# Kernel tuning notes

Measured on AMD Instinct MI355X. Metric: run time of the kernel, lower is better.

The kernel has to match this reference:

```python
import jax, jax.numpy as jnp
import numpy as np

B, S, D = 2, 2048, 2048
H, KVH, HD = 16, 4, 128
E, TOPK, FF = 8, 2, 4096
EPS = 1e-6
THETA = 1000000.0


def setup_inputs() -> dict:
    key = jax.random.key(0)
    ks = jax.random.split(key, 12)
    s = 0.02
    return {
        'hidden_states': jax.random.normal(ks[0], (B, S, D), jnp.float32),
        'attention_mask': jnp.ones((B, S), dtype=bool),
        'wq': jax.random.normal(ks[1], (D, H * HD), jnp.float32) * s,
        'wk': jax.random.normal(ks[2], (D, KVH * HD), jnp.float32) * s,
        'wv': jax.random.normal(ks[3], (D, KVH * HD), jnp.float32) * s,
        'wo': jax.random.normal(ks[4], (H * HD, D), jnp.float32) * s,
        'ln1_w': jnp.ones((D,), jnp.float32),
        'ln2_w': jnp.ones((D,), jnp.float32),
        'gate_w': jax.random.normal(ks[5], (D, E), jnp.float32) * s,
        'w_gate': jax.random.normal(ks[6], (E, D, FF), jnp.float32) * s,
        'w_up': jax.random.normal(ks[7], (E, D, FF), jnp.float32) * s,
        'w_down': jax.random.normal(ks[8], (E, FF, D), jnp.float32) * s,
    }


def rms_norm(x, w):
    xf = x.astype(jnp.float32)
    var = jnp.mean(jnp.square(xf), axis=-1, keepdims=True)
    return w * (xf * jax.lax.rsqrt(var + EPS)).astype(x.dtype)


def rotate_half(x):
    x1, x2 = x[..., : x.shape[-1] // 2], x[..., x.shape[-1] // 2 :]
    return jnp.concatenate((-x2, x1), axis=-1)


def attention(x, mask, wq, wk, wv, wo):
    q = (x @ wq).reshape(B, S, H, HD)
    k = (x @ wk).reshape(B, S, KVH, HD)
    v = (x @ wv).reshape(B, S, KVH, HD)
    # RoPE (fp32 freqs, as in MixtralRotaryEmbedding)
    inv_freq = 1.0 / (THETA ** (jnp.arange(0, HD, 2, dtype=jnp.float32) / HD))
    freqs = jnp.arange(S, dtype=jnp.float32)[:, None] * inv_freq[None, :]  # [S, HD/2]
    emb = jnp.concatenate([freqs, freqs], axis=-1)  # [S, HD]
    cos = jnp.cos(emb)[None, :, None, :]  # [1,S,1,HD]
    sin = jnp.sin(emb)[None, :, None, :]
    q = q * cos + rotate_half(q) * sin
    k = k * cos + rotate_half(k) * sin
    # GQA: repeat kv heads
    k = jnp.repeat(k, H // KVH, axis=2)
    v = jnp.repeat(v, H // KVH, axis=2)
    # faithful to source: keep-mask is triu(ones, k=1) (strictly-above-diagonal)
    causal = jnp.triu(jnp.ones((S, S), dtype=bool), k=1)
    combined = mask[:, None, None, :] & causal[None, None, :, :]  # [B,1,S,S]
    neg = jnp.finfo(jnp.float32).min
    bias = jnp.where(combined, 0.0, neg).astype(jnp.float32)
    scores = jnp.einsum('bqhd,bkhd->bhqk', q, k) * (HD ** -0.5) + bias
    attn = jax.nn.softmax(scores, axis=-1)
    out = jnp.einsum('bhqk,bkhd->bqhd', attn, v).reshape(B, S, H * HD)
    return out @ wo


def moe(x, gate_w, w_gate, w_up, w_down):
    # x: [T, D]
    T = x.shape[0]
    logits = x.astype(jnp.float32) @ gate_w  # fp32 router, [T, E]
    rw = jax.nn.softmax(logits, axis=-1)
    top_w, top_i = jax.lax.top_k(rw, TOPK)
    top_w = top_w / jnp.sum(top_w, axis=-1, keepdims=True)
    w_full = jnp.zeros((T, E), jnp.float32).at[jnp.arange(T)[:, None], top_i].set(top_w)
    out = jnp.zeros_like(x)
    for e in range(E):  # small fixed expert loop
        h = jax.nn.silu(x @ w_gate[e]) * (x @ w_up[e])
        out = out + w_full[:, e, None] * (h @ w_down[e])
    return out


def reference(hidden_states, attention_mask, wq, wk, wv, wo, ln1_w, ln2_w, gate_w, w_gate, w_up, w_down):
    residual = hidden_states
    h = rms_norm(hidden_states, ln1_w)
    h = residual + attention(h, attention_mask, wq, wk, wv, wo)
    residual = h
    h = rms_norm(h, ln2_w)
    m = moe(h.reshape(-1, D), gate_w, w_gate, w_up, w_down).reshape(B, S, D)
    return residual + m
```

## Files before the change

kernel.cpp:

```cpp
#include <hip/hip_runtime.h>
#include <cstdint>
#include <cstddef>


typedef unsigned short u16;
typedef __attribute__((ext_vector_type(8))) short short8;
typedef __attribute__((ext_vector_type(8))) _Float16 half8;
typedef __attribute__((ext_vector_type(8))) __bf16 bf16x8;
typedef __attribute__((ext_vector_type(4))) float f32x4;
typedef __attribute__((ext_vector_type(4))) u16 us4;
typedef __attribute__((ext_vector_type(4))) unsigned int u32x4;

__device__ __forceinline__ u16 f2bf(float f) {
  unsigned u = __builtin_bit_cast(unsigned, f);
  u += 0x7fffu + ((u >> 16) & 1u);
  return (u16)(u >> 16);
}
__device__ __forceinline__ void splitf16(float x, float scale, u16 &hi, u16 &lo) {
  float xs = x * scale;
  _Float16 h = (_Float16)xs;
  hi = __builtin_bit_cast(u16, h);
  _Float16 l = (_Float16)(xs - (float)h);
  lo = __builtin_bit_cast(u16, l);
}
__device__ __forceinline__ f32x4 mma_bf(short8 a, short8 b, f32x4 c) {
  return __builtin_amdgcn_mfma_f32_16x16x32_bf16(
      __builtin_bit_cast(bf16x8, a), __builtin_bit_cast(bf16x8, b), c, 0, 0, 0);
}
__device__ __forceinline__ f32x4 mma_h(short8 a, short8 b, f32x4 c) {
  return __builtin_amdgcn_mfma_f32_16x16x32_f16(
      __builtin_bit_cast(half8, a), __builtin_bit_cast(half8, b), c, 0, 0, 0);
}
__device__ __forceinline__ void gl16(const u16 *g, u16 *l) {
  __builtin_amdgcn_global_load_lds(
      (const __attribute__((address_space(1))) unsigned *)g,
      (__attribute__((address_space(3))) unsigned *)l, 16, 0, 0);
}

template <int OM>
__global__ __launch_bounds__(256) void k_trans(
    const float *__restrict__ src, u16 *__restrict__ d0, u16 *__restrict__ d1,
    int ld_src, int ld_dst, long long zhi, long long zlo, int zmod,
    long long dstz, int inter, float scale) {
  int z = blockIdx.z;
  src += (long long)(z / zmod) * zhi + (long long)(z % zmod) * zlo;
  d0 += (long long)z * dstz;
  if constexpr (OM == 1) d1 += (long long)z * dstz;
  int r0 = blockIdx.y * 64, c0 = blockIdx.x * 64;
  __shared__ float t[64][65];
  int tx = threadIdx.x;
  int rr = tx >> 4, cc = (tx & 15) * 4;
#pragma unroll
  for (int i = 0; i < 4; i++) {
    float4 v = *(const float4 *)(src + (size_t)(r0 + rr + i * 16) * ld_src + c0 + cc);
    t[rr + i * 16][cc] = v.x; t[rr + i * 16][cc + 1] = v.y;
    t[rr + i * 16][cc + 2] = v.z; t[rr + i * 16][cc + 3] = v.w;
  }
  __syncthreads();
#pragma unroll
  for (int i = 0; i < 4; i++) {
    int c = rr + i * 16;
    int f = c0 + c;
    int drow = (inter < 0) ? f : (((f >> 5) << 6) + (f & 31) + (inter << 5));
    size_t bo = (size_t)drow * ld_dst + r0 + cc;
    if constexpr (OM == 0) {
      us4 o;
#pragma unroll
      for (int j = 0; j < 4; j++) o[j] = f2bf(t[cc + j][c]);
      *(us4 *)(d0 + bo) = o;
    } else {
      us4 oh, ol;
#pragma unroll
      for (int j = 0; j < 4; j++) {
        u16 a, b; splitf16(t[cc + j][c], scale, a, b);
        oh[j] = a; ol[j] = b;
      }
      *(us4 *)(d0 + bo) = oh;
      *(us4 *)(d1 + bo) = ol;
    }
  }
}

__global__ __launch_bounds__(256) void k_rms(
    const float *__restrict__ x, const float *__restrict__ w,
    u16 *__restrict__ oh, u16 *__restrict__ ol, float scale16) {
  int row = blockIdx.x, tid = threadIdx.x;
  const float *xr = x + (size_t)row * 2048;
  float4 v0 = *(const float4 *)(xr + tid * 8);
  float4 v1 = *(const float4 *)(xr + tid * 8 + 4);
  float ss = v0.x * v0.x + v0.y * v0.y + v0.z * v0.z + v0.w * v0.w +
             v1.x * v1.x + v1.y * v1.y + v1.z * v1.z + v1.w * v1.w;
  __shared__ float red[256];
  red[tid] = ss;
  __syncthreads();
  for (int s = 128; s > 0; s >>= 1) {
    if (tid < s) red[tid] += red[tid + s];
    __syncthreads();
  }
  float sc = rsqrtf(red[0] * (1.0f / 2048.0f) + 1e-6f);
  float4 w0 = *(const float4 *)(w + tid * 8);
  float4 w1 = *(const float4 *)(w + tid * 8 + 4);
  float o[8] = {v0.x * sc * w0.x, v0.y * sc * w0.y, v0.z * sc * w0.z, v0.w * sc * w0.w,
                v1.x * sc * w1.x, v1.y * sc * w1.y, v1.z * sc * w1.z, v1.w * sc * w1.w};
  size_t bo = (size_t)row * 2048 + tid * 8;
  if (ol) {
    us4 h0, h1, l0, l1;
#pragma unroll
    for (int j = 0; j < 4; j++) {
      u16 a, b;
      splitf16(o[j], scale16, a, b); h0[j] = a; l0[j] = b;
      splitf16(o[j + 4], scale16, a, b); h1[j] = a; l1[j] = b;
    }
    *(us4 *)(oh + bo) = h0; *(us4 *)(oh + bo + 4) = h1;
    *(us4 *)(ol + bo) = l0; *(us4 *)(ol + bo + 4) = l1;
  } else {
    us4 a, b;
#pragma unroll
    for (int j = 0; j < 4; j++) { a[j] = f2bf(o[j]); b[j] = f2bf(o[j + 4]); }
    *(us4 *)(oh + bo) = a; *(us4 *)(oh + bo + 4) = b;
  }
}

__global__ void k_cs(float2 *__restrict__ cs) {
  int idx = blockIdx.x * 256 + threadIdx.x;
  int s = idx >> 6, i = idx & 63;
  double inv = exp2(-(double)i * (19.931568569324174 / 64.0));
  double ang = (double)s * inv;
  cs[idx] = make_float2((float)cos(ang), (float)sin(ang));
}

__global__ __launch_bounds__(256) void k_rope(
    const float *__restrict__ qkv, const float2 *__restrict__ cs,
    u16 *__restrict__ qh, u16 *__restrict__ ql,
    u16 *__restrict__ kh, u16 *__restrict__ kl) {
  int t = blockIdx.x, tid = threadIdx.x;
  int s = t & 2047;
  const float *bp = qkv + (size_t)t * 3072;
  for (int p = tid; p < 1024; p += 256) {
    int hh = p >> 6, i = p & 63;
    float2 c = cs[s * 64 + i];
    float x1 = bp[hh * 128 + i], x2 = bp[hh * 128 + 64 + i];
    float o1 = x1 * c.x - x2 * c.y, o2 = x2 * c.x + x1 * c.y;
    size_t b1 = (size_t)t * 2048 + hh * 128 + i;
    u16 a, b;
    splitf16(o1, 16.f, a, b); qh[b1] = a; ql[b1] = b;
    splitf16(o2, 16.f, a, b); qh[b1 + 64] = a; ql[b1 + 64] = b;
  }
  {
    int hh = tid >> 6, i = tid & 63;
    float2 c = cs[s * 64 + i];
    float x1 = bp[2048 + hh * 128 + i], x2 = bp[2048 + hh * 128 + 64 + i];
    float o1 = x1 * c.x - x2 * c.y, o2 = x2 * c.x + x1 * c.y;
    size_t b1 = (size_t)t * 512 + hh * 128 + i;
    u16 a, b;
    splitf16(o1, 16.f, a, b); kh[b1] = a; kl[b1] = b;
    splitf16(o2, 16.f, a, b); kh[b1 + 64] = a; kl[b1 + 64] = b;
  }
}

__global__ __launch_bounds__(256) void k_attn(
    const u16 *__restrict__ qh, const u16 *__restrict__ ql,
    const u16 *__restrict__ kh, const u16 *__restrict__ kl,
    const u16 *__restrict__ vh, const u16 *__restrict__ vl,
    u16 *__restrict__ oh, u16 *__restrict__ ol) {
  const int qt = blockIdx.x, kvh = blockIdx.y, b = blockIdx.z;
  const int q0 = qt * 16;
  const int tid = threadIdx.x, wid = tid >> 6, lane = tid & 63;
  const int h = kvh * 4 + wid;
  const int lr = lane & 15, g = lane >> 4, lk = g * 8;
  const float SC = 0.08838834764831845f * 1.44269504088896341f / 256.0f;

  __shared__ alignas(16) u16 KT[2][2][4096];
  __shared__ alignas(16) u16 VT[2][2][4096];
  __shared__ alignas(16) u16 Pb[4][2][512];

  short8 qfh[4], qfl[4];
  {
    size_t qo = (size_t)(b * 2048 + q0 + lr) * 2048 + h * 128 + lk;
#pragma unroll
    for (int c = 0; c < 4; c++) {
      qfh[c] = *(const short8 *)(qh + qo + c * 32);
      qfl[c] = *(const short8 *)(ql + qo + c * 32);
    }
  }
  f32x4 accO[8] = {};
  float m_r[4], l_r[4];
#pragma unroll
  for (int r = 0; r < 4; r++) { m_r[r] = -3.0e38f; l_r[r] = 0.f; }

  const int kv_start = (q0 == 2032) ? 0 : (((q0 + 1) >> 5) << 5);
  const int nIter = (2048 - kv_start) >> 5;

  const u16 *khp = kh + (size_t)(b * 2048) * 512 + kvh * 128;
  const u16 *klp = kl + (size_t)(b * 2048) * 512 + kvh * 128;
  const u16 *vhp = vh + ((size_t)(b * 4 + kvh) * 128) * 2048;
  const u16 *vlp = vl + ((size_t)(b * 4 + kvh) * 128) * 2048;

  auto stage = [&](int bf, int kv0) {
#pragma unroll
    for (int j = 0; j < 2; j++) {
      const int c0 = wid * 128 + j * 64;
      const int cc = c0 + lane;
      const int krow = cc >> 4, kcol = (cc & 15) ^ (krow & 7);
      const size_t kg = (size_t)(kv0 + krow) * 512 + kcol * 8;
      gl16(khp + kg, &KT[bf][0][c0 * 8]);
      gl16(klp + kg, &KT[bf][1][c0 * 8]);
      const int vd = cc >> 2, vi = (cc & 3) ^ (vd & 3);
      const size_t vg = (size_t)vd * 2048 + kv0 + vi * 8;
      gl16(vhp + vg, &VT[bf][0][c0 * 8]);
      gl16(vlp + vg, &VT[bf][1][c0 * 8]);
    }
  };

  stage(0, kv_start);
  __syncthreads();
  int buf = 0;
  for (int it = 0; it < nIter; it++) {
    const int kv0 = kv_start + (it << 5);
    if (it + 1 < nIter) stage(buf ^ 1, kv0 + 32);
    f32x4 s0 = {}, s1 = {};
    {
      const u16 *KhL = KT[buf][0], *KlL = KT[buf][1];
#pragma unroll
      for (int c = 0; c < 4; c++) {
        const int idx0 = lr * 128 + (((c * 4 + g) ^ (lr & 7)) << 3);
        const int idx1 = idx0 + 2048;
        short8 k0h = *(const short8 *)(KhL + idx0);
        short8 k0l = *(const short8 *)(KlL + idx0);
        short8 k1h = *(const short8 *)(KhL + idx1);
        short8 k1l = *(const short8 *)(KlL + idx1);
        s0 = mma_h(qfh[c], k0h, s0); s0 = mma_h(qfh[c], k0l, s0); s0 = mma_h(qfl[c], k0h, s0);
        s1 = mma_h(qfh[c], k1h, s1); s1 = mma_h(qfh[c], k1l, s1); s1 = mma_h(qfl[c], k1h, s1);
      }
    }
    const bool msk = (kv0 <= q0 + 15);
    float alpha[4];
#pragma unroll
    for (int r = 0; r < 4; r++) {
      float v0 = s0[r] * SC, v1 = s1[r] * SC;
      if (msk) {
        int rowq = q0 + g * 4 + r;
        if (kv0 + lr <= rowq) v0 = -3.0e38f;
        if (kv0 + 16 + lr <= rowq) v1 = -3.0e38f;
      }
      float mx = fmaxf(v0, v1);
#pragma unroll
      for (int o = 1; o < 16; o <<= 1) mx = fmaxf(mx, __shfl_xor(mx, o));
      float mn = fmaxf(m_r[r], mx);
      float p0 = exp2f(v0 - mn), p1 = exp2f(v1 - mn);
      float sum = p0 + p1;
#pragma unroll
      for (int o = 1; o < 16; o <<= 1) sum += __shfl_xor(sum, o);
      alpha[r] = exp2f(m_r[r] - mn);
      l_r[r] = l_r[r] * alpha[r] + sum;
      m_r[r] = mn;
      const int prow = g * 4 + r;
      {
        int c0l = lr, c1l = 16 + lr;
        int p0i = prow * 32 + ((c0l & 7) | ((((c0l >> 3) ^ g) & 3) << 3));
        int p1i = prow * 32 + ((c1l & 7) | ((((c1l >> 3) ^ g) & 3) << 3));
        u16 x, y;
        splitf16(p0, 16.f, x, y); Pb[wid][0][p0i] = x; Pb[wid][1][p0i] = y;
        splitf16(p1, 16.f, x, y); Pb[wid][0][p1i] = x; Pb[wid][1][p1i] = y;
      }
    }
#pragma unroll
    for (int nt = 0; nt < 8; nt++) {
      f32x4 t = accO[nt];
      t[0] *= alpha[0]; t[1] *= alpha[1]; t[2] *= alpha[2]; t[3] *= alpha[3];
      accO[nt] = t;
    }
    asm volatile("s_waitcnt lgkmcnt(0)" ::: "memory");
    const int pidx = lr * 32 + (((g ^ (lr >> 2)) & 3) << 3);
    short8 pfh = *(const short8 *)(&Pb[wid][0][pidx]);
    short8 pfl = *(const short8 *)(&Pb[wid][1][pidx]);
    {
      const u16 *VhL = VT[buf][0], *VlL = VT[buf][1];
#pragma unroll
      for (int nt = 0; nt < 8; nt++) {
        const int d = nt * 16 + lr;
        const int vidx = d * 32 + (((g ^ (d & 3)) & 3) << 3);
        short8 wfh = *(const short8 *)(VhL + vidx);
        short8 wfl = *(const short8 *)(VlL + vidx);
        f32x4 t = accO[nt];
        t = mma_h(pfh, wfh, t); t = mma_h(pfh, wfl, t); t = mma_h(pfl, wfh, t);
        accO[nt] = t;
      }
    }
    __syncthreads();
    buf ^= 1;
  }
  float inv[4];
#pragma unroll
  for (int r = 0; r < 4; r++) inv[r] = 1.0f / (l_r[r] * 256.0f);
#pragma unroll
  for (int nt = 0; nt < 8; nt++)
#pragma unroll
    for (int r = 0; r < 4; r++) {
      float v = accO[nt][r] * inv[r];
      size_t idx = (size_t)(b * 2048 + q0 + g * 4 + r) * 2048 + h * 128 + nt * 16 + lr;
      u16 x, y; splitf16(v, 16.f, x, y);
      oh[idx] = x; ol[idx] = y;
    }
}

template <int MODE>
__global__ __launch_bounds__(256) void k_gemm(
    const u16 *__restrict__ Ah, const u16 *__restrict__ Al,
    const u16 *__restrict__ Bh, const u16 *__restrict__ Bl,
    int M, int N, int K, int lda, int ldb, int ldc, float descale,
    float *__restrict__ outf, const float *__restrict__ resid) {
  const int tid = threadIdx.x;
  const int wid = tid >> 6, lane = tid & 63;
  const int wr = wid >> 1, wc = wid & 1;
  const int l15 = lane & 15, l4 = lane >> 4;
  const int n0 = blockIdx.x * 128, m0 = blockIdx.y * 128;
  __shared__ alignas(16) u16 AsH[4096], BsH[4096];
  __shared__ alignas(16) u16 AsL[4096], BsL[4096];
  const int r16 = lane >> 2, c8 = (lane & 3) << 3;
  int a0 = m0 + wid * 16 + r16, a1 = a0 + 64;
  const u16 *pa0 = Ah + (size_t)a0 * lda + c8;
  const u16 *pa1 = Ah + (size_t)a1 * lda + c8;
  const int b0 = n0 + wid * 16 + r16, b1 = b0 + 64;
  const u16 *pb0 = Bh + (size_t)b0 * ldb + c8;
  const u16 *pb1 = Bh + (size_t)b1 * ldb + c8;
  const u16 *qa0 = Al + (size_t)a0 * lda + c8;
  const u16 *qa1 = Al + (size_t)a1 * lda + c8;
  const u16 *qb0 = Bl + (size_t)b0 * ldb + c8;
  const u16 *qb1 = Bl + (size_t)b1 * ldb + c8;
  u16 *sa0 = AsH + wid * 512, *sa1 = AsH + 2048 + wid * 512;
  u16 *sb0 = BsH + wid * 512, *sb1 = BsH + 2048 + wid * 512;
  f32x4 acc[4][4] = {};
  const int fa = (wr * 64 + l15) * 32 + (l4 << 3);
  const int fb = (wc * 64 + l15) * 32 + (l4 << 3);
  for (int k0 = 0; k0 < K; k0 += 32) {
    gl16(pa0 + k0, sa0); gl16(pa1 + k0, sa1);
    gl16(pb0 + k0, sb0); gl16(pb1 + k0, sb1);
    gl16(qa0 + k0, AsL + wid * 512); gl16(qa1 + k0, AsL + 2048 + wid * 512);
    gl16(qb0 + k0, BsL + wid * 512); gl16(qb1 + k0, BsL + 2048 + wid * 512);
    __syncthreads();
    short8 ah[4], bh[4], al[4], bl[4];
#pragma unroll
    for (int i = 0; i < 4; i++) ah[i] = *(const short8 *)(AsH + fa + i * 512);
#pragma unroll
    for (int i = 0; i < 4; i++) bh[i] = *(const short8 *)(BsH + fb + i * 512);
#pragma unroll
    for (int i = 0; i < 4; i++) al[i] = *(const short8 *)(AsL + fa + i * 512);
#pragma unroll
    for (int i = 0; i < 4; i++) bl[i] = *(const short8 *)(BsL + fb + i * 512);
#pragma unroll
    for (int mi = 0; mi < 4; mi++)
#pragma unroll
      for (int ni = 0; ni < 4; ni++) {
        f32x4 c = acc[mi][ni];
        c = mma_h(ah[mi], bh[ni], c);
        c = mma_h(ah[mi], bl[ni], c);
        c = mma_h(al[mi], bh[ni], c);
        acc[mi][ni] = c;
      }
    __syncthreads();
  }
#pragma unroll
  for (int mi = 0; mi < 4; mi++)
#pragma unroll
    for (int q = 0; q < 4; q++) {
      int row = m0 + wr * 64 + l4 * 4 + mi * 16 + q;
      size_t rb = (size_t)row * ldc;
#pragma unroll
      for (int ni = 0; ni < 4; ni++) {
        int col = n0 + wc * 64 + ni * 16 + l15;
        float v = acc[mi][ni][q] * descale;
        if constexpr (MODE == 1) v += resid[rb + col];
        outf[rb + col] = v;
      }
    }
}

template <int MODE>
__global__ __launch_bounds__(512, 1) void k_gemm8(
    const u16 *__restrict__ A, const u16 *__restrict__ Ball,
    int N, int K, int lda, int ldb, int ldc,
    float *__restrict__ outf, u16 *__restrict__ outh,
    const int *__restrict__ offs, const int *__restrict__ counts,
    const int *__restrict__ row_token, const float *__restrict__ row_w) {
  const int e = blockIdx.z;
  const int seg = offs[e], cnt = counts[e];
  const int m0 = blockIdx.y * 256;
  if (m0 >= cnt) return;
  const int n0 = blockIdx.x * 256;
  const u16 *B = Ball + (size_t)e * (size_t)N * (size_t)ldb;
  const int tid = threadIdx.x, wid = tid >> 6, lane = tid & 63;
  const int wr = wid >> 2, wc = wid & 3;
  const int l15 = lane & 15, l4 = lane >> 4;

  __shared__ alignas(16) u16 Ls[4][2][8192];

  const u16 *pA[2], *pB[2];
#pragma unroll
  for (int j = 0; j < 2; j++) {
    int s = (wid * 2 + j) * 64 + lane;
    int row = s >> 2;
    int kc = (s & 3) ^ ((row >> 1) & 3);
    int ra = m0 + row; if (ra > cnt - 1) ra = cnt - 1;
    pA[j] = A + (size_t)(seg + ra) * lda + kc * 8;
    pB[j] = B + (size_t)(n0 + row) * ldb + kc * 8;
  }
  int offA[8], offB[4];
#pragma unroll
  for (int mi = 0; mi < 8; mi++) {
    int r = wr * 128 + mi * 16 + l15;
    offA[mi] = (r * 4 + (l4 ^ ((r >> 1) & 3))) << 3;
  }
#pragma unroll
  for (int ni = 0; ni < 4; ni++) {
    int r = wc * 64 + ni * 16 + l15;
    offB[ni] = (r * 4 + (l4 ^ ((r >> 1) & 3))) << 3;
  }

  f32x4 acc[8][4] = {};
  const int nT = K >> 5;
  auto stage = [&](int t, int j) {
    gl16(pA[j] + (t << 5), &Ls[t & 3][0][(wid * 2 + j) << 9]);
    gl16(pB[j] + (t << 5), &Ls[t & 3][1][(wid * 2 + j) << 9]);
  };
  stage(0, 0); stage(0, 1); stage(1, 0); stage(1, 1);
  asm volatile("s_waitcnt vmcnt(4)" ::: "memory");
  __builtin_amdgcn_sched_barrier(0);
  __builtin_amdgcn_s_barrier();
  __builtin_amdgcn_sched_barrier(0);

  short8 bf[4], af0[4], af1[4];
  for (int t = 0; t < nT; t++) {
    const u16 *LA = &Ls[t & 3][0][0], *LB = &Ls[t & 3][1][0];
#pragma unroll
    for (int i = 0; i < 4; i++) bf[i] = *(const short8 *)(LB + offB[i]);
#pragma unroll
    for (int i = 0; i < 4; i++) af0[i] = *(const short8 *)(LA + offA[i]);
    if (t + 2 < nT) stage(t + 2, 0);
    asm volatile("s_waitcnt lgkmcnt(0)" ::: "memory");
    __builtin_amdgcn_sched_barrier(0);
    __builtin_amdgcn_s_setprio(1);
#pragma unroll
    for (int mi = 0; mi < 4; mi++)
#pragma unroll
      for (int ni = 0; ni < 4; ni++)
        acc[mi][ni] = mma_bf(af0[mi], bf[ni], acc[mi][ni]);
    __builtin_amdgcn_s_setprio(0);
#pragma unroll
    for (int i = 0; i < 4; i++) af1[i] = *(const short8 *)(LA + offA[4 + i]);
    if (t + 2 < nT) stage(t + 2, 1);
    asm volatile("s_waitcnt lgkmcnt(0)" ::: "memory");
    __builtin_amdgcn_sched_barrier(0);
    __builtin_amdgcn_s_setprio(1);
#pragma unroll
    for (int mi = 0; mi < 4; mi++)
#pragma unroll
      for (int ni = 0; ni < 4; ni++)
        acc[4 + mi][ni] = mma_bf(af1[mi], bf[ni], acc[4 + mi][ni]);
    __builtin_amdgcn_s_setprio(0);
    if (t + 1 < nT) {
      if (t + 2 < nT) {
        asm volatile("s_waitcnt vmcnt(4)" ::: "memory");
      } else {
        asm volatile("s_waitcnt vmcnt(0)" ::: "memory");
      }
      __builtin_amdgcn_sched_barrier(0);
      __builtin_amdgcn_s_barrier();
      __builtin_amdgcn_sched_barrier(0);
    }
  }

  if constexpr (MODE == 2) {
    const int f0 = (n0 + wc * 64) >> 1;
#pragma unroll
    for (int mi = 0; mi < 8; mi++)
#pragma unroll
      for (int q = 0; q < 4; q++) {
        int rl = m0 + wr * 128 + mi * 16 + l4 * 4 + q;
        if (rl < cnt) {
          size_t rb = (size_t)(seg + rl) * ldc;
#pragma unroll
          for (int nt = 0; nt < 2; nt++) {
            float g = acc[mi][nt][q], u = acc[mi][nt + 2][q];
            float hv = (g / (1.0f + __expf(-g))) * u;
            outh[rb + f0 + nt * 16 + l15] = f2bf(hv);
          }
        }
      }
  } else {
#pragma unroll
    for (int mi = 0; mi < 8; mi++)
#pragma unroll
      for (int q = 0; q < 4; q++) {
        int rl = m0 + wr * 128 + mi * 16 + l4 * 4 + q;
        if (rl < cnt) {
          int tok = row_token[seg + rl];
          float w = row_w[seg + rl];
          size_t rb = (size_t)tok * ldc;
#pragma unroll
          for (int ni = 0; ni < 4; ni++)
            atomicAdd(outf + rb + n0 + wc * 64 + ni * 16 + l15,
                      w * acc[mi][ni][q]);
        }
      }
  }
}

__global__ __launch_bounds__(64) void k_router(
    const float *__restrict__ hb, const float *__restrict__ w2,
    const float *__restrict__ gw, int *__restrict__ topi,
    float *__restrict__ topw, int *__restrict__ counts) {
  const int t = blockIdx.x, lane = threadIdx.x;
  const float *xr = hb + (size_t)t * 2048;
  float xs[32];
  float ss = 0.f;
#pragma unroll
  for (int c = 0; c < 8; c++) {
    float4 v = *(const float4 *)(xr + c * 256 + lane * 4);
    xs[c * 4 + 0] = v.x; xs[c * 4 + 1] = v.y; xs[c * 4 + 2] = v.z; xs[c * 4 + 3] = v.w;
    ss += v.x * v.x + v.y * v.y + v.z * v.z + v.w * v.w;
  }
#pragma unroll
  for (int o = 1; o < 64; o <<= 1) ss += __shfl_xor(ss, o);
  const float sc = rsqrtf(ss * (1.0f / 2048.0f) + 1e-6f);
  float acc[8] = {0, 0, 0, 0, 0, 0, 0, 0};
#pragma unroll
  for (int c = 0; c < 8; c++)
#pragma unroll
    for (int j = 0; j < 4; j++) {
      int d = c * 256 + lane * 4 + j;
      float xn = xs[c * 4 + j] * sc * w2[d];
      float4 g0 = *(const float4 *)(gw + (size_t)d * 8);
      float4 g1 = *(const float4 *)(gw + (size_t)d * 8 + 4);
      acc[0] += xn * g0.x; acc[1] += xn * g0.y; acc[2] += xn * g0.z; acc[3] += xn * g0.w;
      acc[4] += xn * g1.x; acc[5] += xn * g1.y; acc[6] += xn * g1.z; acc[7] += xn * g1.w;
    }
#pragma unroll
  for (int e = 0; e < 8; e++) {
    float v = acc[e];
#pragma unroll
    for (int o = 1; o < 64; o <<= 1) v += __shfl_xor(v, o);
    acc[e] = v;
  }
  if (lane == 0) {
    float mx = acc[0];
#pragma unroll
    for (int e = 1; e < 8; e++) mx = fmaxf(mx, acc[e]);
    float p[8];
#pragma unroll
    for (int e = 0; e < 8; e++) p[e] = __expf(acc[e] - mx);
    int e0 = 0;
#pragma unroll
    for (int e = 1; e < 8; e++) if (p[e] > p[e0]) e0 = e;
    int e1 = (e0 == 0) ? 1 : 0;
#pragma unroll
    for (int e = 0; e < 8; e++) if (e != e0 && p[e] > p[e1]) e1 = e;
    float s2 = p[e0] + p[e1];
    topi[t * 2] = e0; topi[t * 2 + 1] = e1;
    topw[t * 2] = p[e0] / s2; topw[t * 2 + 1] = p[e1] / s2;
    atomicAdd(counts + e0, 1);
    atomicAdd(counts + e1, 1);
  }
}

__global__ void k_zero(int *__restrict__ p) {
  if (threadIdx.x < 8) p[threadIdx.x] = 0;
}
__global__ void k_offsets(const int *__restrict__ counts, int *__restrict__ offs,
                          int *__restrict__ cursors) {
  if (threadIdx.x == 0) {
    int o = 0;
    for (int e = 0; e < 8; e++) { offs[e] = o; o += counts[e]; cursors[e] = 0; }
    offs[8] = o;
  }
}
__global__ __launch_bounds__(256) void k_scatter(
    const int *__restrict__ topi, const float *__restrict__ topw,
    const int *__restrict__ offs, int *__restrict__ cursors,
    int *__restrict__ row_token, float *__restrict__ row_w) {
  int t = blockIdx.x * 256 + threadIdx.x;
  if (t >= 4096) return;
#pragma unroll
  for (int s = 0; s < 2; s++) {
    int e = topi[t * 2 + s];
    int pos = offs[e] + atomicAdd(cursors + e, 1);
    row_token[pos] = t;
    row_w[pos] = topw[t * 2 + s];
  }
}
__global__ __launch_bounds__(256) void k_gather(
    const u16 *__restrict__ h2, const int *__restrict__ row_token,
    u16 *__restrict__ xg) {
  int r = blockIdx.x;
  int t = row_token[r];
  ((u32x4 *)(xg + (size_t)r * 2048))[threadIdx.x] =
      ((const u32x4 *)(h2 + (size_t)t * 2048))[threadIdx.x];
}

extern "C" void kernel_launch(void *const *d_in, const int *in_sizes, int n_in,
                              void *d_out, int out_size, void *d_ws,
                              size_t ws_size, hipStream_t stream) {
  const float *hidden = (const float *)d_in[0];
  const float *wq = (const float *)d_in[2];
  const float *wk = (const float *)d_in[3];
  const float *wv = (const float *)d_in[4];
  const float *wo = (const float *)d_in[5];
  const float *ln1 = (const float *)d_in[6];
  const float *ln2 = (const float *)d_in[7];
  const float *gw = (const float *)d_in[8];
  const float *wg = (const float *)d_in[9];
  const float *wu = (const float *)d_in[10];
  const float *wd = (const float *)d_in[11];
  float *out = (float *)d_out;

  char *base = (char *)d_ws;
  size_t off = 0;
  auto alloc = [&](size_t bytes) -> char * {
    char *p = base + off;
    off += (bytes + 255) & ~(size_t)255;
    return p;
  };
  u16 *wqkvTh = (u16 *)alloc((size_t)3072 * 2048 * 2);
  u16 *wqkvTl = (u16 *)alloc((size_t)3072 * 2048 * 2);
  u16 *woTh = (u16 *)alloc((size_t)2048 * 2048 * 2);
  u16 *woTl = (u16 *)alloc((size_t)2048 * 2048 * 2);
  u16 *wguT = (u16 *)alloc((size_t)8 * 8192 * 2048 * 2);
  u16 *wdT = (u16 *)alloc((size_t)8 * 2048 * 4096 * 2);
  u16 *h1h = (u16 *)alloc((size_t)4096 * 2048 * 2);
  u16 *h1l = (u16 *)alloc((size_t)4096 * 2048 * 2);
  float *qkv = (float *)alloc((size_t)4096 * 3072 * 4);
  u16 *qbh = (u16 *)alloc((size_t)4096 * 2048 * 2);
  u16 *qbl = (u16 *)alloc((size_t)4096 * 2048 * 2);
  u16 *kbh = (u16 *)alloc((size_t)4096 * 512 * 2);
  u16 *kbl = (u16 *)alloc((size_t)4096 * 512 * 2);
  u16 *vth = (u16 *)alloc((size_t)8 * 128 * 2048 * 2);
  u16 *vtl = (u16 *)alloc((size_t)8 * 128 * 2048 * 2);
  float2 *cs = (float2 *)alloc((size_t)2048 * 64 * 8);
  u16 *aoh = (u16 *)alloc((size_t)4096 * 2048 * 2);
  u16 *aol = (u16 *)alloc((size_t)4096 * 2048 * 2);
  u16 *h2 = (u16 *)alloc((size_t)4096 * 2048 * 2);
  int *topi = (int *)alloc(4096 * 2 * 4);
  float *topwt = (float *)alloc(4096 * 2 * 4);
  int *counts = (int *)alloc(64 * 4);
  int *offs = (int *)alloc(64 * 4);
  int *cursors = (int *)alloc(64 * 4);
  int *row_token = (int *)alloc(8192 * 4);
  float *row_w = (float *)alloc(8192 * 4);
  u16 *xg = (u16 *)alloc((size_t)8192 * 2048 * 2);
  u16 *Hb = (u16 *)alloc((size_t)8192 * 4096 * 2);
  if (off > ws_size) return;

  dim3 T256(256), T64(64);
  k_cs<<<dim3(512), T256, 0, stream>>>(cs);
  k_trans<1><<<dim3(32, 32, 1), T256, 0, stream>>>(wq, wqkvTh, wqkvTl, 2048, 2048, 0, 0, 1, 0, -1, 256.f);
  k_trans<1><<<dim3(8, 32, 1), T256, 0, stream>>>(wk, wqkvTh + (size_t)2048 * 2048, wqkvTl + (size_t)2048 * 2048, 512, 2048, 0, 0, 1, 0, -1, 256.f);
  k_trans<1><<<dim3(8, 32, 1), T256, 0, stream>>>(wv, wqkvTh + (size_t)2560 * 2048, wqkvTl + (size_t)2560 * 2048, 512, 2048, 0, 0, 1, 0, -1, 256.f);
  k_trans<1><<<dim3(32, 32, 1), T256, 0, stream>>>(wo, woTh, woTl, 2048, 2048, 0, 0, 1, 0, -1, 256.f);
  k_trans<0><<<dim3(64, 32, 8), T256, 0, stream>>>(wg, wguT, nullptr, 4096, 2048, (long long)2048 * 4096, 0, 1, (long long)8192 * 2048, 0, 1.f);
  k_trans<0><<<dim3(64, 32, 8), T256, 0, stream>>>(wu, wguT, nullptr, 4096, 2048, (long long)2048 * 4096, 0, 1, (long long)8192 * 2048, 1, 1.f);
  k_trans<0><<<dim3(32, 64, 8), T256, 0, stream>>>(wd, wdT, nullptr, 2048, 4096, (long long)4096 * 2048, 0, 1, (long long)2048 * 4096, -1, 1.f);
  k_rms<<<dim3(4096), T256, 0, stream>>>(hidden, ln1, h1h, h1l, 16.f);
  k_gemm<0><<<dim3(24, 32, 1), T256, 0, stream>>>(
      h1h, h1l, wqkvTh, wqkvTl, 4096, 3072, 2048, 2048, 2048, 3072,
      1.f / 4096.f, qkv, nullptr);
  k_rope<<<dim3(4096), T256, 0, stream>>>(qkv, cs, qbh, qbl, kbh, kbl);
  k_trans<1><<<dim3(2, 32, 8), T256, 0, stream>>>(qkv + 2560, vth, vtl, 3072, 2048, (long long)2048 * 3072, 128, 4, (long long)128 * 2048, -1, 16.f);
  k_attn<<<dim3(128, 4, 2), T256, 0, stream>>>(qbh, qbl, kbh, kbl, vth, vtl, aoh, aol);
  k_gemm<1><<<dim3(16, 32, 1), T256, 0, stream>>>(
      aoh, aol, woTh, woTl, 4096, 2048, 2048, 2048, 2048, 2048,
      1.f / 4096.f, out, hidden);
  k_rms<<<dim3(4096), T256, 0, stream>>>(out, ln2, h2, nullptr, 1.f);
  k_zero<<<dim3(1), T64, 0, stream>>>(counts);
  k_router<<<dim3(4096), T64, 0, stream>>>(out, ln2, gw, topi, topwt, counts);
  k_offsets<<<dim3(1), dim3(1), 0, stream>>>(counts, offs, cursors);
  k_scatter<<<dim3(16), T256, 0, stream>>>(topi, topwt, offs, cursors, row_token, row_w);
  k_gather<<<dim3(8192), T256, 0, stream>>>(h2, row_token, xg);
  k_gemm8<2><<<dim3(32, 16, 8), dim3(512), 0, stream>>>(
      xg, wguT, 8192, 2048, 2048, 2048, 4096,
      nullptr, Hb, offs, counts, nullptr, nullptr);
  k_gemm8<3><<<dim3(8, 16, 8), dim3(512), 0, stream>>>(
      Hb, wdT, 2048, 4096, 4096, 4096, 2048,
      out, nullptr, offs, counts, row_token, row_w);
  (void)in_sizes; (void)n_in; (void)out_size;
}
```

Before: 1.646 ms.

## Double attention query tile to 32 rows with 8 waves and add last-row fixup kernel

The attention kernel now processes 32 query rows per block using 512 threads, so each staged K/V tile is shared by twice as many waves and the number of blocks is halved. Query tiles are traversed in reverse order for the second batch to spread the triangular work more evenly. The fully masked last row (which becomes a uniform average of V) is split out into a separate small kernel that computes the mean of V directly. This cuts redundant K/V loads per query but doubles registers and LDS pressure per block and adds a launch.

```diff
diff --git a/kernel.cpp b/kernel.cpp
--- a/kernel.cpp
+++ b/kernel.cpp
@@ -158,25 +158,27 @@
   }
 }
 
-__global__ __launch_bounds__(256) void k_attn(
+__global__ __launch_bounds__(512, 4) void k_attn(
     const u16 *__restrict__ qh, const u16 *__restrict__ ql,
     const u16 *__restrict__ kh, const u16 *__restrict__ kl,
     const u16 *__restrict__ vh, const u16 *__restrict__ vl,
     u16 *__restrict__ oh, u16 *__restrict__ ol) {
-  const int qt = blockIdx.x, kvh = blockIdx.y, b = blockIdx.z;
-  const int q0 = qt * 16;
+  const int qx = blockIdx.x, kvh = blockIdx.y, b = blockIdx.z;
+  const int qt = (b == 0) ? qx : 63 - qx;
+  const int q0 = qt * 32;
   const int tid = threadIdx.x, wid = tid >> 6, lane = tid & 63;
-  const int h = kvh * 4 + wid;
+  const int hq = wid & 3, rh = wid >> 2;
+  const int h = kvh * 4 + hq;
   const int lr = lane & 15, g = lane >> 4, lk = g * 8;
   const float SC = 0.08838834764831845f * 1.44269504088896341f / 256.0f;
 
   __shared__ alignas(16) u16 KT[2][2][4096];
   __shared__ alignas(16) u16 VT[2][2][4096];
-  __shared__ alignas(16) u16 Pb[4][2][512];
+  __shared__ alignas(16) u16 Pb[8][2][512];
 
   short8 qfh[4], qfl[4];
   {
-    size_t qo = (size_t)(b * 2048 + q0 + lr) * 2048 + h * 128 + lk;
+    size_t qo = (size_t)(b * 2048 + q0 + rh * 16 + lr) * 2048 + h * 128 + lk;
 #pragma unroll
     for (int c = 0; c < 4; c++) {
       qfh[c] = *(const short8 *)(qh + qo + c * 32);
@@ -188,7 +190,7 @@
 #pragma unroll
   for (int r = 0; r < 4; r++) { m_r[r] = -3.0e38f; l_r[r] = 0.f; }
 
-  const int kv_start = (q0 == 2032) ? 0 : (((q0 + 1) >> 5) << 5);
+  const int kv_start = q0;
   const int nIter = (2048 - kv_start) >> 5;
 
   const u16 *khp = kh + (size_t)(b * 2048) * 512 + kvh * 128;
@@ -197,19 +199,16 @@
   const u16 *vlp = vl + ((size_t)(b * 4 + kvh) * 128) * 2048;
 
   auto stage = [&](int bf, int kv0) {
-#pragma unroll
-    for (int j = 0; j < 2; j++) {
-      const int c0 = wid * 128 + j * 64;
-      const int cc = c0 + lane;
-      const int krow = cc >> 4, kcol = (cc & 15) ^ (krow & 7);
-      const size_t kg = (size_t)(kv0 + krow) * 512 + kcol * 8;
-      gl16(khp + kg, &KT[bf][0][c0 * 8]);
-      gl16(klp + kg, &KT[bf][1][c0 * 8]);
-      const int vd = cc >> 2, vi = (cc & 3) ^ (vd & 3);
-      const size_t vg = (size_t)vd * 2048 + kv0 + vi * 8;
-      gl16(vhp + vg, &VT[bf][0][c0 * 8]);
-      gl16(vlp + vg, &VT[bf][1][c0 * 8]);
-    }
+    const int c0 = wid * 64;
+    const int cc = tid;
+    const int krow = cc >> 4, kcol = (cc & 15) ^ (krow & 7);
+    const size_t kg = (size_t)(kv0 + krow) * 512 + kcol * 8;
+    gl16(khp + kg, &KT[bf][0][c0 * 8]);
+    gl16(klp + kg, &KT[bf][1][c0 * 8]);
+    const int vd = cc >> 2, vi = (cc & 3) ^ (vd & 3);
+    const size_t vg = (size_t)vd * 2048 + kv0 + vi * 8;
+    gl16(vhp + vg, &VT[bf][0][c0 * 8]);
+    gl16(vlp + vg, &VT[bf][1][c0 * 8]);
   };
 
   stage(0, kv_start);
@@ -233,13 +232,13 @@
         s1 = mma_h(qfh[c], k1h, s1); s1 = mma_h(qfh[c], k1l, s1); s1 = mma_h(qfl[c], k1h, s1);
       }
     }
-    const bool msk = (kv0 <= q0 + 15);
+    const bool msk = (kv0 <= q0 + 31);
     float alpha[4];
 #pragma unroll
     for (int r = 0; r < 4; r++) {
       float v0 = s0[r] * SC, v1 = s1[r] * SC;
       if (msk) {
-        int rowq = q0 + g * 4 + r;
+        int rowq = q0 + rh * 16 + g * 4 + r;
         if (kv0 + lr <= rowq) v0 = -3.0e38f;
         if (kv0 + 16 + lr <= rowq) v1 = -3.0e38f;
       }
@@ -298,10 +297,44 @@
 #pragma unroll
     for (int r = 0; r < 4; r++) {
       float v = accO[nt][r] * inv[r];
-      size_t idx = (size_t)(b * 2048 + q0 + g * 4 + r) * 2048 + h * 128 + nt * 16 + lr;
+      size_t idx = (size_t)(b * 2048 + q0 + rh * 16 + g * 4 + r) * 2048 + h * 128 + nt * 16 + lr;
       u16 x, y; splitf16(v, 16.f, x, y);
       oh[idx] = x; ol[idx] = y;
     }
+}
+
+__global__ __launch_bounds__(256) void k_fixrow(
+    const u16 *__restrict__ vh, const u16 *__restrict__ vl,
+    u16 *__restrict__ oh, u16 *__restrict__ ol) {
+  const int bg = blockIdx.x >> 4, dg = blockIdx.x & 15;
+  const int tid = threadIdx.x, lane = tid & 63, w = tid >> 6;
+  __shared__ float part[4][8];
+#pragma unroll
+  for (int i = 0; i < 8; i++) {
+    size_t ro = ((size_t)(bg * 128 + dg * 8 + i)) * 2048 + tid * 8;
+    short8 a = *(const short8 *)(vh + ro);
+    short8 c = *(const short8 *)(vl + ro);
+    float s = 0.f;
+#pragma unroll
+    for (int j = 0; j < 8; j++)
+      s += (float)__builtin_bit_cast(_Float16, (u16)a[j]) +
+           (float)__builtin_bit_cast(_Float16, (u16)c[j]);
+#pragma unroll
+    for (int o = 1; o < 64; o <<= 1) s += __shfl_xor(s, o);
+    if (lane == 0) part[w][i] = s;
+  }
+  __syncthreads();
+  if (tid < 8) {
+    float tot = part[0][tid] + part[1][tid] + part[2][tid] + part[3][tid];
+    float v = tot * (1.0f / 32768.0f);
+    u16 x, y; splitf16(v, 16.f, x, y);
+    int bb = bg >> 2, kvh = bg & 3;
+#pragma unroll
+    for (int hq2 = 0; hq2 < 4; hq2++) {
+      size_t idx = ((size_t)(bb * 2048 + 2047)) * 2048 + (kvh * 4 + hq2) * 128 + dg * 8 + tid;
+      oh[idx] = x; ol[idx] = y;
+    }
+  }
 }
 
 template <int MODE>
@@ -665,7 +698,8 @@
       1.f / 4096.f, qkv, nullptr);
   k_rope<<<dim3(4096), T256, 0, stream>>>(qkv, cs, qbh, qbl, kbh, kbl);
   k_trans<1><<<dim3(2, 32, 8), T256, 0, stream>>>(qkv + 2560, vth, vtl, 3072, 2048, (long long)2048 * 3072, 128, 4, (long long)128 * 2048, -1, 16.f);
-  k_attn<<<dim3(128, 4, 2), T256, 0, stream>>>(qbh, qbl, kbh, kbl, vth, vtl, aoh, aol);
+  k_attn<<<dim3(64, 4, 2), dim3(512), 0, stream>>>(qbh, qbl, kbh, kbl, vth, vtl, aoh, aol);
+  k_fixrow<<<dim3(128), T256, 0, stream>>>(vth, vtl, aoh, aol);
   k_gemm<1><<<dim3(16, 32, 1), T256, 0, stream>>>(
       aoh, aol, woTh, woTl, 4096, 2048, 2048, 2048, 2048, 2048,
       1.f / 4096.f, out, hidden);
```

Measured after the change: 1.523 ms. 7.5% less time.
